# Performance work log

Hardware: AMD Instinct MI355X
Metric: run time of the kernel (lower is better)

The kernel has to match this reference:

```python
import jax, jax.numpy as jnp
import numpy as np

# ---- static config (MaskedViTConfig, eval mode with inference_topk) ----
B, IMG, P, C = 32, 224, 16, 3
G = IMG // P            # 14
N = G * G + 1           # 197 tokens incl cls
D, NH = 768, 12
HD = D // NH            # 64
SCALE = HD ** -0.5
HID = 4 * D             # 3072
GH = 128                # gate hidden
WARM, DYN = 2, 10
TOPK = 118              # min(inference_topk, N-1)
NC = 1000
EPS_MASK = 1e-6
LN_EPS = 1e-5


def _ln(x, g, b):
    mu = x.mean(-1, keepdims=True)
    var = ((x - mu) ** 2).mean(-1, keepdims=True)
    return (x - mu) / jnp.sqrt(var + LN_EPS) * g + b


def _attn(x, qkv_w, qkv_b, proj_w, proj_b, add_mask):
    # x: [B,N,D]; add_mask: [B,N] additive logit bias per key, or None
    Bb, Nn, _ = x.shape
    qkv = (x @ qkv_w + qkv_b).reshape(Bb, Nn, 3, NH, HD)
    q, k, v = qkv[:, :, 0], qkv[:, :, 1], qkv[:, :, 2]  # [B,N,H,hd]
    attn = jnp.einsum('bqhd,bkhd->bhqk', q, k) * SCALE
    if add_mask is not None:
        attn = attn + add_mask[:, None, None, :]
    attn = jax.nn.softmax(attn, axis=-1)
    out = jnp.einsum('bhqk,bkhd->bqhd', attn, v).reshape(Bb, Nn, D)
    return out @ proj_w + proj_b


def _mlp(x, w1, b1, w2, b2):
    return jax.nn.gelu(x @ w1 + b1, approximate=False) @ w2 + b2


def setup_inputs() -> dict:
    key = jax.random.key(0)
    ks = iter(jax.random.split(key, 64))
    nrm = lambda shape, s=0.02: jax.random.normal(next(ks), shape, jnp.float32) * s
    z = lambda *shape: jnp.zeros(shape, jnp.float32)
    o = lambda *shape: jnp.ones(shape, jnp.float32)
    inp = {
        'images': jax.random.normal(next(ks), (B, C, IMG, IMG), jnp.float32),
        'patch_w': nrm((D, C, P, P)), 'patch_b': z(D),
        'cls_token': nrm((1, 1, D)), 'pos_embed': nrm((1, N, D)),
        # warmup blocks, stacked on leading axis [WARM,...]
        'w_ln1_g': o(WARM, D), 'w_ln1_b': z(WARM, D),
        'w_qkv_w': nrm((WARM, D, 3 * D)), 'w_qkv_b': z(WARM, 3 * D),
        'w_proj_w': nrm((WARM, D, D)), 'w_proj_b': z(WARM, D),
        'w_ln2_g': o(WARM, D), 'w_ln2_b': z(WARM, D),
        'w_fc1_w': nrm((WARM, D, HID)), 'w_fc1_b': z(WARM, HID),
        'w_fc2_w': nrm((WARM, HID, D)), 'w_fc2_b': z(WARM, D),
        # dynamic masked blocks [DYN,...]
        'd_ln1_g': o(DYN, D), 'd_ln1_b': z(DYN, D),
        'd_qkv_w': nrm((DYN, D, 3 * D)), 'd_qkv_b': z(DYN, 3 * D),
        'd_proj_w': nrm((DYN, D, D)), 'd_proj_b': z(DYN, D),
        'd_ln2_g': o(DYN, D), 'd_ln2_b': z(DYN, D),
        'd_fc1_w': nrm((DYN, D, HID)), 'd_fc1_b': z(DYN, HID),
        'd_fc2_w': nrm((DYN, HID, D)), 'd_fc2_b': z(DYN, D),
        # gate predictor: LayerNorm -> Linear(D,GH) -> GELU -> Linear(GH,1)
        'd_gln_g': o(DYN, D), 'd_gln_b': z(DYN, D),
        'd_gw1': nrm((DYN, D, GH)), 'd_gb1': z(DYN, GH),
        'd_gw2': nrm((DYN, GH, 1)), 'd_gb2': z(DYN, 1),
        # final norm + head
        'norm_g': o(D), 'norm_b': z(D),
        'head_w': nrm((D, NC)), 'head_b': z(NC),
    }
    return inp


def reference(images, patch_w, patch_b, cls_token, pos_embed,
              w_ln1_g, w_ln1_b, w_qkv_w, w_qkv_b, w_proj_w, w_proj_b,
              w_ln2_g, w_ln2_b, w_fc1_w, w_fc1_b, w_fc2_w, w_fc2_b,
              d_ln1_g, d_ln1_b, d_qkv_w, d_qkv_b, d_proj_w, d_proj_b,
              d_ln2_g, d_ln2_b, d_fc1_w, d_fc1_b, d_fc2_w, d_fc2_b,
              d_gln_g, d_gln_b, d_gw1, d_gb1, d_gw2, d_gb2,
              norm_g, norm_b, head_w, head_b):
    Bb = images.shape[0]
    # patch embed: conv with kernel==stride==P is a block reshape + matmul
    x6 = images.reshape(Bb, C, G, P, G, P)
    x = jnp.einsum('bcxpyq,dcpq->bxyd', x6, patch_w).reshape(Bb, G * G, D) + patch_b
    cls = jnp.broadcast_to(cls_token, (Bb, 1, D))
    x = jnp.concatenate([cls, x], axis=1) + pos_embed  # [B,N,D]

    for i in range(WARM):
        x = x + _attn(_ln(x, w_ln1_g[i], w_ln1_b[i]),
                      w_qkv_w[i], w_qkv_b[i], w_proj_w[i], w_proj_b[i], None)
        x = x + _mlp(_ln(x, w_ln2_g[i], w_ln2_b[i]),
                     w_fc1_w[i], w_fc1_b[i], w_fc2_w[i], w_fc2_b[i])

    for j in range(DYN):
        # gate predictor -> logits [B,N]; cls forced kept
        h = _ln(x, d_gln_g[j], d_gln_b[j])
        logits = (jax.nn.gelu(h @ d_gw1[j] + d_gb1[j], approximate=False)
                  @ d_gw2[j] + d_gb2[j]).squeeze(-1)
        logits = logits.at[:, 0].set(1e9)
        # eval-mode top-k keep mask (inference_topk path)
        _, idx = jax.lax.top_k(logits[:, 1:], TOPK)
        m = jnp.zeros_like(logits).at[:, 0].set(1.0)
        m = m.at[jnp.arange(Bb)[:, None], idx + 1].set(1.0)
        add_mask = jnp.log(jnp.clip(m, EPS_MASK, 1.0))
        x = x + _attn(_ln(x, d_ln1_g[j], d_ln1_b[j]),
                      d_qkv_w[j], d_qkv_b[j], d_proj_w[j], d_proj_b[j], add_mask)
        v = _mlp(_ln(x, d_ln2_g[j], d_ln2_b[j]),
                 d_fc1_w[j], d_fc1_b[j], d_fc2_w[j], d_fc2_b[j])
        x = x + v * m[:, :, None]  # gate_mlp_updates=True

    x = _ln(x, norm_g, norm_b)
    return x[:, 0] @ head_w + head_b  # [B, num_classes]
```

## Files before the change

### kernel.cpp

```cpp
#include <hip/hip_runtime.h>
#include <hip/hip_bf16.h>
#include <math.h>


typedef __bf16 bf16_t;
typedef __attribute__((ext_vector_type(8))) __bf16 bf16x8;
typedef __attribute__((ext_vector_type(4))) float f32x4;

#define DI __device__ __forceinline__

constexpr int NB     = 32;
constexpr int NTOK   = 197;
constexpr int DMODEL = 768;
constexpr int NHEAD  = 12;
constexpr int HDIM   = 64;
constexpr int HIDN   = 3072;
constexpr int GHID   = 128;
constexpr int MROWS  = NB * NTOK;
constexpr int PROWS  = NB * 196;
constexpr int NSEL   = 119;
constexpr int MROWSC = NB * NSEL;
constexpr int NLAYER = 12;
constexpr int KTOP   = 118;
constexpr float ATT_SCALE = 0.125f;
constexpr float LNEPS  = 1e-5f;

DI f32x4 mfma16(bf16x8 a, bf16x8 b, f32x4 c) {
    return __builtin_amdgcn_mfma_f32_16x16x32_bf16(a, b, c, 0, 0, 0);
}

DI void gld_lds16(const void* g, void* l) {
    __builtin_amdgcn_global_load_lds(
        (__attribute__((address_space(1))) void*)(g),
        (__attribute__((address_space(3))) void*)(l), 16, 0, 0);
}

enum { EP_BF16 = 0, EP_GELU = 1, EP_RES = 2, EP_F32 = 4 };

template<int MODE, bool GA, bool SC, bool AT, int BN>
__global__ __launch_bounds__(256)
void gemm_bf16(const bf16_t* __restrict__ A, const bf16_t* __restrict__ Wt,
               const float* __restrict__ bias, void* __restrict__ Cout,
               float* __restrict__ resid, const int* __restrict__ rowidx,
               int M, int N, int K, int ldc, int klen)
{
    constexpr int WN = BN / 2;
    constexpr int NF = WN / 16;
    __shared__ __align__(16) bf16_t As[2][128 * 32];
    __shared__ __align__(16) bf16_t Bs[2][BN * 32];
    const int tid  = threadIdx.x;
    const int lane = tid & 63;
    const int wave = tid >> 6;
    const int wm = wave >> 1, wn = wave & 1;
    const int quad = lane >> 4, l16 = lane & 15;
    const int m0 = blockIdx.y * 128;
    const int n0 = blockIdx.x * BN;
    const int koff = AT ? blockIdx.z * klen : 0;

    f32x4 zero4 = {0.f, 0.f, 0.f, 0.f};
    f32x4 acc[4][NF];
#pragma unroll
    for (int i = 0; i < 4; ++i)
#pragma unroll
        for (int j = 0; j < NF; ++j) acc[i][j] = zero4;

    const int rh  = tid >> 2;
    const int seg = tid & 3;
    int cA0 = min(m0 + rh,      M - 1);
    int cA1 = min(m0 + 64 + rh, M - 1);
    const int rA0 = GA ? rowidx[cA0] : cA0;
    const int rA1 = GA ? rowidx[cA1] : cA1;
    const int rB0 = min(n0 + rh, N - 1);
    const int rB1 = (BN == 128) ? min(n0 + 64 + rh, N - 1) : 0;
    const bf16_t* pA0 = A  + (size_t)rA0 * K + koff + seg * 8;
    const bf16_t* pA1 = A  + (size_t)rA1 * K + koff + seg * 8;
    const bf16_t* pB0 = Wt + (size_t)rB0 * K + koff + seg * 8;
    const bf16_t* pB1 = Wt + (size_t)rB1 * K + koff + seg * 8;
    const int lofs0 = wave * 512;
    const int lofs1 = 2048 + wave * 512;

    auto stage = [&](int kt2, int buf) {
        const int kb = kt2 << 5;
        gld_lds16(pA0 + kb, As[buf] + lofs0);
        gld_lds16(pA1 + kb, As[buf] + lofs1);
        gld_lds16(pB0 + kb, Bs[buf] + lofs0);
        if (BN == 128) gld_lds16(pB1 + kb, Bs[buf] + lofs1);
    };

    const int nkt = klen >> 5;
    stage(0, 0);
    stage(1, 1);

    for (int kt = 0; kt < nkt; ++kt) {
        const int cur = kt & 1;
        if (kt + 1 < nkt) {
            if constexpr (BN == 128) asm volatile("s_waitcnt vmcnt(4)" ::: "memory");
            else                     asm volatile("s_waitcnt vmcnt(3)" ::: "memory");
        } else {
            asm volatile("s_waitcnt vmcnt(0)" ::: "memory");
        }
        __builtin_amdgcn_s_barrier();

        bf16x8 af[4], bfr[NF];
#pragma unroll
        for (int i = 0; i < 4; ++i)
            af[i] = *reinterpret_cast<const bf16x8*>(As[cur] + (wm * 64 + i * 16 + l16) * 32 + quad * 8);
#pragma unroll
        for (int j = 0; j < NF; ++j)
            bfr[j] = *reinterpret_cast<const bf16x8*>(Bs[cur] + (wn * WN + j * 16 + l16) * 32 + quad * 8);

        asm volatile("s_waitcnt lgkmcnt(0)" ::: "memory");
        __builtin_amdgcn_sched_barrier(0);
        __builtin_amdgcn_s_barrier();

        if (kt + 2 < nkt) stage(kt + 2, cur);

#pragma unroll
        for (int i = 0; i < 4; ++i)
#pragma unroll
            for (int j = 0; j < NF; ++j)
                acc[i][j] = mfma16(af[i], bfr[j], acc[i][j]);
    }

    const bool addb = bias && (!AT || blockIdx.z == 0);
#pragma unroll
    for (int j = 0; j < NF; ++j) {
        int c = n0 + wn * WN + j * 16 + l16;
        if (c >= N) continue;
        float bj = addb ? bias[c] : 0.f;
#pragma unroll
        for (int i = 0; i < 4; ++i) {
#pragma unroll
            for (int r = 0; r < 4; ++r) {
                int mr = m0 + wm * 64 + i * 16 + quad * 4 + r;
                if (mr >= M) continue;
                float v = acc[i][j][r] + bj;
                int orow = SC ? rowidx[mr] : mr;
                size_t off = (size_t)orow * ldc + c;
                if (MODE == EP_BF16) {
                    ((bf16_t*)Cout)[off] = (bf16_t)v;
                } else if (MODE == EP_GELU) {
                    float g = 0.5f * v * (1.f + erff(v * 0.70710678118f));
                    ((bf16_t*)Cout)[off] = (bf16_t)g;
                } else if (MODE == EP_F32) {
                    ((float*)Cout)[off] = v;
                } else {
                    if (AT) atomicAdd(&resid[off], v);
                    else    resid[off] += v;
                }
            }
        }
    }
}

DI float block_reduce_sum(float val, float* sh) {
#pragma unroll
    for (int off = 32; off; off >>= 1) val += __shfl_down(val, off, 64);
    __syncthreads();
    if ((threadIdx.x & 63) == 0) sh[threadIdx.x >> 6] = val;
    __syncthreads();
    return sh[0] + sh[1] + sh[2] + sh[3];
}

template<typename OUT>
__global__ __launch_bounds__(256)
void ln_kernel(const float* __restrict__ X, const float* __restrict__ g,
               const float* __restrict__ bta, OUT* __restrict__ H, int row_mul)
{
    __shared__ float sh[4];
    const int t = threadIdx.x;
    const float* xr = X + (size_t)blockIdx.x * row_mul * DMODEL;
    float v[3];
#pragma unroll
    for (int i = 0; i < 3; ++i) v[i] = xr[t + i * 256];
    float s = v[0] + v[1] + v[2];
    s = block_reduce_sum(s, sh);
    float mu = s * (1.f / DMODEL);
    float q = 0.f;
#pragma unroll
    for (int i = 0; i < 3; ++i) { float d = v[i] - mu; q += d * d; }
    q = block_reduce_sum(q, sh);
    float rstd = rsqrtf(q * (1.f / DMODEL) + LNEPS);
    OUT* hr = H + (size_t)blockIdx.x * DMODEL;
#pragma unroll
    for (int i = 0; i < 3; ++i) {
        int c = t + i * 256;
        hr[c] = (OUT)((v[i] - mu) * rstd * g[c] + bta[c]);
    }
}

__global__ __launch_bounds__(256)
void ln_dual_kernel(const float* __restrict__ X,
                    const float* __restrict__ g1, const float* __restrict__ b1,
                    const float* __restrict__ g2, const float* __restrict__ b2,
                    float* __restrict__ H1, bf16_t* __restrict__ H2)
{
    __shared__ float sh[4];
    const int t = threadIdx.x;
    const float* xr = X + (size_t)blockIdx.x * DMODEL;
    float v[3];
#pragma unroll
    for (int i = 0; i < 3; ++i) v[i] = xr[t + i * 256];
    float s = v[0] + v[1] + v[2];
    s = block_reduce_sum(s, sh);
    float mu = s * (1.f / DMODEL);
    float q = 0.f;
#pragma unroll
    for (int i = 0; i < 3; ++i) { float d = v[i] - mu; q += d * d; }
    q = block_reduce_sum(q, sh);
    float rstd = rsqrtf(q * (1.f / DMODEL) + LNEPS);
    float* h1 = H1 + (size_t)blockIdx.x * DMODEL;
    bf16_t* h2 = H2 + (size_t)blockIdx.x * DMODEL;
#pragma unroll
    for (int i = 0; i < 3; ++i) {
        int c = t + i * 256;
        float nrm = (v[i] - mu) * rstd;
        h1[c] = nrm * g1[c] + b1[c];
        h2[c] = (bf16_t)(nrm * g2[c] + b2[c]);
    }
}

template<bool COMPACT>
__global__ __launch_bounds__(256)
void attn_kernel(const bf16_t* __restrict__ qkv,
                 const int* __restrict__ rowidx,
                 bf16_t* __restrict__ outp)
{
    constexpr int NV  = COMPACT ? NSEL : NTOK;
    constexpr int NK  = COMPACT ? 128 : 224;
    constexpr int NKT = COMPACT ? 8 : 13;
    constexpr int NKS = NK / 32;
    constexpr int KP  = NK + 8;
    __shared__ __align__(16) bf16_t Vt[64 * KP];
    __shared__ __align__(16) bf16_t Ps[4][16 * KP];
    const int b = blockIdx.z, h = blockIdx.y, qt = blockIdx.x;
    const int tid = threadIdx.x, wave = tid >> 6, lane = tid & 63;
    const int quad = lane >> 4, l16 = lane & 15;

    {
        int d = tid & 63, ng = tid >> 6;
        for (int n = ng; n < NK; n += 4) {
            bf16_t v = (bf16_t)0.f;
            if (n < NV) {
                size_t row = COMPACT ? (size_t)rowidx[b * NSEL + n]
                                     : (size_t)b * NTOK + n;
                v = qkv[(row * 3 + 2) * DMODEL + h * HDIM + d];
            }
            Vt[d * KP + n] = v;
        }
    }
    __syncthreads();

    const int qbase = qt * 64 + wave * 16;
    const int qrow = qbase + l16;
    const int qc = qrow < 196 ? qrow : 196;
    bf16x8 aq[2];
#pragma unroll
    for (int t = 0; t < 2; ++t)
        aq[t] = *reinterpret_cast<const bf16x8*>(
            qkv + (((size_t)b * NTOK + qc) * 3 + 0) * DMODEL + h * HDIM + t * 32 + quad * 8);

    float sreg[NKT][4];
#pragma unroll
    for (int kt = 0; kt < NKT; ++kt) {
        int key = kt * 16 + l16;
        int kc = key < NV ? key : NV - 1;
        size_t krow = COMPACT ? (size_t)rowidx[b * NSEL + kc]
                              : (size_t)b * NTOK + kc;
        const bf16_t* kb = qkv + (krow * 3 + 1) * DMODEL + h * HDIM;
        bf16x8 kf0 = *reinterpret_cast<const bf16x8*>(kb + quad * 8);
        bf16x8 kf1 = *reinterpret_cast<const bf16x8*>(kb + 32 + quad * 8);
        f32x4 s = {0.f, 0.f, 0.f, 0.f};
        s = mfma16(aq[0], kf0, s);
        s = mfma16(aq[1], kf1, s);
        bool kvalid = key < NV;
#pragma unroll
        for (int r = 0; r < 4; ++r)
            sreg[kt][r] = kvalid ? (s[r] * ATT_SCALE) : -1e30f;
    }

    float psum[4];
#pragma unroll
    for (int r = 0; r < 4; ++r) {
        float mx = -1e30f;
#pragma unroll
        for (int kt = 0; kt < NKT; ++kt) mx = fmaxf(mx, sreg[kt][r]);
#pragma unroll
        for (int d = 1; d < 16; d <<= 1) mx = fmaxf(mx, __shfl_xor(mx, d, 64));
        float sum = 0.f;
#pragma unroll
        for (int kt = 0; kt < NKT; ++kt) {
            float p = expf(sreg[kt][r] - mx);
            sreg[kt][r] = p;
            sum += p;
        }
#pragma unroll
        for (int d = 1; d < 16; d <<= 1) sum += __shfl_xor(sum, d, 64);
        psum[r] = sum;
    }

#pragma unroll
    for (int kt = 0; kt < NKT; ++kt)
#pragma unroll
        for (int r = 0; r < 4; ++r)
            Ps[wave][(quad * 4 + r) * KP + kt * 16 + l16] = (bf16_t)sreg[kt][r];
    if (!COMPACT) {
        int rr = lane & 15, c0 = 208 + (lane >> 4) * 4;
#pragma unroll
        for (int i = 0; i < 4; ++i) Ps[wave][rr * KP + c0 + i] = (bf16_t)0.f;
    }
    __syncthreads();

    f32x4 o[4];
#pragma unroll
    for (int j = 0; j < 4; ++j) o[j] = (f32x4){0.f, 0.f, 0.f, 0.f};
#pragma unroll
    for (int ks = 0; ks < NKS; ++ks) {
        bf16x8 ap = *reinterpret_cast<const bf16x8*>(&Ps[wave][l16 * KP + ks * 32 + quad * 8]);
#pragma unroll
        for (int j = 0; j < 4; ++j) {
            bf16x8 vf = *reinterpret_cast<const bf16x8*>(&Vt[(j * 16 + l16) * KP + ks * 32 + quad * 8]);
            o[j] = mfma16(ap, vf, o[j]);
        }
    }

#pragma unroll
    for (int r = 0; r < 4; ++r) {
        int q = qbase + quad * 4 + r;
        if (q < 197) {
            float rs = 1.f / fmaxf(psum[r], 1e-20f);
#pragma unroll
            for (int j = 0; j < 4; ++j)
                outp[((size_t)b * NTOK + q) * DMODEL + h * HDIM + j * 16 + l16] =
                    (bf16_t)(o[j][r] * rs);
        }
    }
}

__global__ __launch_bounds__(256)
void transpose_f32(const float* __restrict__ src, bf16_t* __restrict__ dst, int K, int N)
{
    __shared__ bf16_t tile[64][65];
    const size_t ls = (size_t)K * N * blockIdx.z;
    int k0 = blockIdx.y * 64, n0 = blockIdx.x * 64;
    int c = threadIdx.x & 63, r0 = threadIdx.x >> 6;
#pragma unroll
    for (int i = 0; i < 16; ++i) {
        int r = r0 + i * 4;
        tile[r][c] = (k0 + r < K && n0 + c < N)
                   ? (bf16_t)src[ls + (size_t)(k0 + r) * N + n0 + c] : (bf16_t)0.f;
    }
    __syncthreads();
#pragma unroll
    for (int i = 0; i < 16; ++i) {
        int r = r0 + i * 4;
        if (n0 + r < N && k0 + c < K) dst[ls + (size_t)(n0 + r) * K + k0 + c] = tile[c][r];
    }
}

__global__ void cvt_f32_bf16(const float* __restrict__ src, bf16_t* __restrict__ dst, int n)
{
    int i = blockIdx.x * 256 + threadIdx.x;
    if (i < n) dst[i] = (bf16_t)src[i];
}

__global__ void im2col_kernel(const float* __restrict__ img, bf16_t* __restrict__ Ap)
{
    int idx = blockIdx.x * 256 + threadIdx.x;
    if (idx >= PROWS * 768) return;
    int col = idx % 768, row = idx / 768;
    int b = row / 196, t = row % 196;
    int gi = t / 14, gj = t % 14;
    int c = col >> 8, rr = col & 255, p = rr >> 4, q = rr & 15;
    Ap[idx] = (bf16_t)img[(((size_t)b * 3 + c) * 224 + gi * 16 + p) * 224 + gj * 16 + q];
}

__global__ void assemble_x(const float* __restrict__ patch, const float* __restrict__ cls,
                           const float* __restrict__ pos, float* __restrict__ X)
{
    int idx = blockIdx.x * 256 + threadIdx.x;
    if (idx >= MROWS * DMODEL) return;
    int d = idx % DMODEL, rest = idx / DMODEL;
    int n = rest % NTOK, b = rest / NTOK;
    float v;
    if (n == 0) v = cls[d] + pos[d];
    else        v = patch[((size_t)b * 196 + (n - 1)) * DMODEL + d] + pos[(size_t)n * DMODEL + d];
    X[idx] = v;
}

__global__ __launch_bounds__(256)
void gate_fused_f32(const float* __restrict__ A, const float* __restrict__ W1,
                    const float* __restrict__ b1, const float* __restrict__ w2,
                    const float* __restrict__ b2, float* __restrict__ logits)
{
    __shared__ __align__(16) float As[16][64];
    __shared__ __align__(16) float Ws[64][128];
    const int tid = threadIdx.x;
    const int m0 = blockIdx.x * 16;
    const int tx = tid & 31;
    const int rg = tid >> 5;
    f32x4 acc0 = {0.f, 0.f, 0.f, 0.f};
    f32x4 acc1 = {0.f, 0.f, 0.f, 0.f};
    for (int k0 = 0; k0 < 768; k0 += 64) {
        __syncthreads();
        {
            int idx = tid * 4;
            int r = idx >> 6, c = idx & 63;
            *reinterpret_cast<f32x4*>(&As[r][c]) =
                *reinterpret_cast<const f32x4*>(&A[(size_t)(m0 + r) * 768 + k0 + c]);
        }
#pragma unroll
        for (int i = 0; i < 8; ++i) {
            int idx = (tid + i * 256) * 4;
            int r = idx >> 7, c = idx & 127;
            *reinterpret_cast<f32x4*>(&Ws[r][c]) =
                *reinterpret_cast<const f32x4*>(&W1[(size_t)(k0 + r) * 128 + c]);
        }
        __syncthreads();
#pragma unroll
        for (int kk = 0; kk < 64; ++kk) {
            float a0 = As[rg * 2 + 0][kk];
            float a1 = As[rg * 2 + 1][kk];
            f32x4 w = *reinterpret_cast<const f32x4*>(&Ws[kk][tx * 4]);
#pragma unroll
            for (int j = 0; j < 4; ++j) {
                acc0[j] += a0 * w[j];
                acc1[j] += a1 * w[j];
            }
        }
    }
    float s0 = 0.f, s1 = 0.f;
#pragma unroll
    for (int j = 0; j < 4; ++j) {
        int c = tx * 4 + j;
        float bj = b1[c], wj = w2[c];
        float v0 = acc0[j] + bj;
        float v1 = acc1[j] + bj;
        s0 += 0.5f * v0 * (1.f + erff(v0 * 0.70710678118f)) * wj;
        s1 += 0.5f * v1 * (1.f + erff(v1 * 0.70710678118f)) * wj;
    }
#pragma unroll
    for (int d = 1; d < 32; d <<= 1) {
        s0 += __shfl_xor(s0, d, 64);
        s1 += __shfl_xor(s1, d, 64);
    }
    if (tx == 0) {
        logits[m0 + rg * 2 + 0] = s0 + b2[0];
        logits[m0 + rg * 2 + 1] = s1 + b2[0];
    }
}

__global__ __launch_bounds__(256)
void topk_kernel(const float* __restrict__ logits, int* __restrict__ rowidx)
{
    __shared__ float ls[196];
    int b = blockIdx.x, t = threadIdx.x;
    if (t < 196) ls[t] = logits[b * NTOK + 1 + t];
    __syncthreads();
    if (t < 196) {
        float li = ls[t];
        int cnt = 0;
        for (int j = 0; j < 196; ++j) {
            float lj = ls[j];
            cnt += (lj > li) || (lj == li && j < t);
        }
        if (cnt < KTOP) rowidx[b * NSEL + 1 + cnt] = b * NTOK + 1 + t;
    }
    if (t == 0) rowidx[b * NSEL] = b * NTOK;
}

__global__ void fill_sentinel(float* out, int n)
{
    int i = blockIdx.x * 256 + threadIdx.x;
    if (i < n) out[i] = 12345.0f;
}

static void launch_gemm(int mode, const bf16_t* A, const bf16_t* Wt, const float* bias,
                        void* C, float* resid,
                        int M, int N, int K, int ldc, hipStream_t s)
{
    dim3 grid((N + 127) / 128, (M + 127) / 128);
    dim3 blk(256);
    switch (mode) {
    case EP_BF16: gemm_bf16<EP_BF16, false, false, false, 128><<<grid, blk, 0, s>>>(A, Wt, bias, C, resid, nullptr, M, N, K, ldc, K); break;
    case EP_GELU: gemm_bf16<EP_GELU, false, false, false, 128><<<grid, blk, 0, s>>>(A, Wt, bias, C, resid, nullptr, M, N, K, ldc, K); break;
    case EP_RES:  gemm_bf16<EP_RES,  false, false, false, 128><<<grid, blk, 0, s>>>(A, Wt, bias, C, resid, nullptr, M, N, K, ldc, K); break;
    case EP_F32:  gemm_bf16<EP_F32,  false, false, false, 128><<<grid, blk, 0, s>>>(A, Wt, bias, C, resid, nullptr, M, N, K, ldc, K); break;
    }
}

static void launch_gemm_res_sk2_n64(const bf16_t* A, const bf16_t* Wt, const float* bias,
                                    float* resid, int M, int N, int K, int ldc, hipStream_t s)
{
    dim3 grid((N + 63) / 64, (M + 127) / 128, 2);
    gemm_bf16<EP_RES, false, false, true, 64><<<grid, 256, 0, s>>>(
        A, Wt, bias, nullptr, resid, nullptr, M, N, K, ldc, K / 2);
}

extern "C" void kernel_launch(void* const* d_in, const int* in_sizes, int n_in,
                              void* d_out, int out_size, void* d_ws, size_t ws_size,
                              hipStream_t stream)
{
    (void)in_sizes; (void)n_in;
    const float* images   = (const float*)d_in[0];
    const float* patch_w  = (const float*)d_in[1];
    const float* patch_b  = (const float*)d_in[2];
    const float* cls_tok  = (const float*)d_in[3];
    const float* pos_emb  = (const float*)d_in[4];
    const float* w_ln1_g  = (const float*)d_in[5];
    const float* w_ln1_b  = (const float*)d_in[6];
    const float* w_qkv_w  = (const float*)d_in[7];
    const float* w_qkv_b  = (const float*)d_in[8];
    const float* w_proj_w = (const float*)d_in[9];
    const float* w_proj_b = (const float*)d_in[10];
    const float* w_ln2_g  = (const float*)d_in[11];
    const float* w_ln2_b  = (const float*)d_in[12];
    const float* w_fc1_w  = (const float*)d_in[13];
    const float* w_fc1_b  = (const float*)d_in[14];
    const float* w_fc2_w  = (const float*)d_in[15];
    const float* w_fc2_b  = (const float*)d_in[16];
    const float* d_ln1_g  = (const float*)d_in[17];
    const float* d_ln1_b  = (const float*)d_in[18];
    const float* d_qkv_w  = (const float*)d_in[19];
    const float* d_qkv_b  = (const float*)d_in[20];
    const float* d_proj_w = (const float*)d_in[21];
    const float* d_proj_b = (const float*)d_in[22];
    const float* d_ln2_g  = (const float*)d_in[23];
    const float* d_ln2_b  = (const float*)d_in[24];
    const float* d_fc1_w  = (const float*)d_in[25];
    const float* d_fc1_b  = (const float*)d_in[26];
    const float* d_fc2_w  = (const float*)d_in[27];
    const float* d_fc2_b  = (const float*)d_in[28];
    const float* d_gln_g  = (const float*)d_in[29];
    const float* d_gln_b  = (const float*)d_in[30];
    const float* d_gw1    = (const float*)d_in[31];
    const float* d_gb1    = (const float*)d_in[32];
    const float* d_gw2    = (const float*)d_in[33];
    const float* d_gb2    = (const float*)d_in[34];
    const float* norm_g   = (const float*)d_in[35];
    const float* norm_b   = (const float*)d_in[36];
    const float* head_w   = (const float*)d_in[37];
    const float* head_b   = (const float*)d_in[38];

    char* wp = (char*)d_ws;
    auto alloc = [&](size_t bytes) -> char* {
        char* p = wp; wp += (bytes + 255) & ~(size_t)255; return p;
    };
    bf16_t* wtqkv  = (bf16_t*)alloc((size_t)NLAYER * 2304 * 768 * 2);
    bf16_t* wtproj = (bf16_t*)alloc((size_t)NLAYER * 768 * 768 * 2);
    bf16_t* wtfc1  = (bf16_t*)alloc((size_t)NLAYER * 3072 * 768 * 2);
    bf16_t* wtfc2  = (bf16_t*)alloc((size_t)NLAYER * 768 * 3072 * 2);
    bf16_t* wthead = (bf16_t*)alloc((size_t)1024 * 768 * 2);
    bf16_t* pwbf   = (bf16_t*)alloc((size_t)768 * 768 * 2);
    float*  x      = (float*)alloc((size_t)MROWS * DMODEL * 4);
    bf16_t* h      = (bf16_t*)alloc((size_t)MROWS * DMODEL * 2);
    float*  hgate  = (float*)alloc((size_t)MROWS * DMODEL * 4);
    bf16_t* hcls   = (bf16_t*)alloc((size_t)NB * DMODEL * 2);
    bf16_t* qkvb   = (bf16_t*)alloc((size_t)MROWS * 2304 * 2);
    bf16_t* attno  = (bf16_t*)alloc((size_t)MROWS * DMODEL * 2);
    bf16_t* hid    = (bf16_t*)alloc((size_t)MROWS * HIDN * 2);
    float*  logits = (float*)alloc((size_t)MROWS * 4);
    int*    rowidx = (int*)alloc((size_t)MROWSC * 4);
    size_t used = (size_t)(wp - (char*)d_ws);
    if (used > ws_size) {
        fill_sentinel<<<(out_size + 255) / 256, 256, 0, stream>>>((float*)d_out, out_size);
        return;
    }
    bf16_t* Ap = hid;
    float* patchout = (float*)((char*)hid + (size_t)PROWS * 768 * 2);

    transpose_f32<<<dim3(36, 12, 2),  256, 0, stream>>>(w_qkv_w,  wtqkv,                      768, 2304);
    transpose_f32<<<dim3(36, 12, 10), 256, 0, stream>>>(d_qkv_w,  wtqkv + (size_t)2*2304*768, 768, 2304);
    transpose_f32<<<dim3(12, 12, 2),  256, 0, stream>>>(w_proj_w, wtproj,                     768, 768);
    transpose_f32<<<dim3(12, 12, 10), 256, 0, stream>>>(d_proj_w, wtproj + (size_t)2*768*768, 768, 768);
    transpose_f32<<<dim3(48, 12, 2),  256, 0, stream>>>(w_fc1_w,  wtfc1,                      768, 3072);
    transpose_f32<<<dim3(48, 12, 10), 256, 0, stream>>>(d_fc1_w,  wtfc1 + (size_t)2*3072*768, 768, 3072);
    transpose_f32<<<dim3(12, 48, 2),  256, 0, stream>>>(w_fc2_w,  wtfc2,                      3072, 768);
    transpose_f32<<<dim3(12, 48, 10), 256, 0, stream>>>(d_fc2_w,  wtfc2 + (size_t)2*768*3072, 3072, 768);
    transpose_f32<<<dim3(16, 12, 1),  256, 0, stream>>>(head_w,   wthead,                     768, 1000);
    cvt_f32_bf16<<<(768 * 768 + 255) / 256, 256, 0, stream>>>(patch_w, pwbf, 768 * 768);

    im2col_kernel<<<(PROWS * 768 + 255) / 256, 256, 0, stream>>>(images, Ap);
    launch_gemm(EP_F32, Ap, pwbf, patch_b, patchout, nullptr,
                PROWS, 768, 768, 768, stream);
    assemble_x<<<(MROWS * DMODEL + 255) / 256, 256, 0, stream>>>(patchout, cls_tok, pos_emb, x);

    for (int L = 0; L < NLAYER; ++L) {
        bool warm = (L < 2);
        int li = warm ? L : (L - 2);
        const float* ln1g = warm ? w_ln1_g + li*768 : d_ln1_g + li*768;
        const float* ln1b = warm ? w_ln1_b + li*768 : d_ln1_b + li*768;
        const float* ln2g = warm ? w_ln2_g + li*768 : d_ln2_g + li*768;
        const float* ln2b = warm ? w_ln2_b + li*768 : d_ln2_b + li*768;
        const float* qkvbias  = warm ? w_qkv_b + li*2304 : d_qkv_b + li*2304;
        const float* projbias = warm ? w_proj_b + li*768 : d_proj_b + li*768;
        const float* fc1bias  = warm ? w_fc1_b + (size_t)li*3072 : d_fc1_b + (size_t)li*3072;
        const float* fc2bias  = warm ? w_fc2_b + li*768 : d_fc2_b + li*768;
        const bf16_t* Wq = wtqkv + (size_t)L * 2304 * 768;
        const bf16_t* Wp = wtproj + (size_t)L * 768 * 768;
        const bf16_t* W1 = wtfc1 + (size_t)L * 3072 * 768;
        const bf16_t* W2 = wtfc2 + (size_t)L * 768 * 3072;

        if (!warm) {
            ln_dual_kernel<<<MROWS, 256, 0, stream>>>(
                x, d_gln_g + li*768, d_gln_b + li*768, ln1g, ln1b, hgate, h);
            gate_fused_f32<<<MROWS / 16, 256, 0, stream>>>(
                hgate, d_gw1 + (size_t)li*768*128, d_gb1 + li*128,
                d_gw2 + (size_t)li*128, d_gb2 + li, logits);
            topk_kernel<<<NB, 256, 0, stream>>>(logits, rowidx);
        } else {
            ln_kernel<bf16_t><<<MROWS, 256, 0, stream>>>(x, ln1g, ln1b, h, 1);
        }
        launch_gemm(EP_BF16, h, Wq, qkvbias, qkvb, nullptr,
                    MROWS, 2304, 768, 2304, stream);
        if (warm)
            attn_kernel<false><<<dim3(4, NHEAD, NB), 256, 0, stream>>>(qkvb, nullptr, attno);
        else
            attn_kernel<true><<<dim3(4, NHEAD, NB), 256, 0, stream>>>(qkvb, rowidx, attno);
        launch_gemm_res_sk2_n64(attno, Wp, projbias, x, MROWS, 768, 768, 768, stream);
        ln_kernel<bf16_t><<<MROWS, 256, 0, stream>>>(x, ln2g, ln2b, h, 1);
        if (warm) {
            launch_gemm(EP_GELU, h, W1, fc1bias, hid, nullptr,
                        MROWS, 3072, 768, 3072, stream);
            launch_gemm_res_sk2_n64(hid, W2, fc2bias, x, MROWS, 768, 3072, 768, stream);
        } else {
            dim3 g1(48, (MROWSC + 127) / 128);
            gemm_bf16<EP_GELU, true, false, false, 64><<<g1, 256, 0, stream>>>(
                h, W1, fc1bias, hid, nullptr, rowidx, MROWSC, 3072, 768, 3072, 768);
            dim3 g2(12, (MROWSC + 127) / 128, 2);
            gemm_bf16<EP_RES, false, true, true, 64><<<g2, 256, 0, stream>>>(
                hid, W2, fc2bias, nullptr, x, rowidx, MROWSC, 768, 3072, 768, 1536);
        }
    }

    ln_kernel<bf16_t><<<NB, 256, 0, stream>>>(x, norm_g, norm_b, hcls, NTOK);
    launch_gemm(EP_F32, hcls, wthead, head_b, d_out, nullptr,
                NB, 1000, 768, 1000, stream);
}
```

Measured before the change: 4.440 ms.

## Remap GEMM workgroups across XCDs and fuse gate LayerNorm into gate kernel

The GEMM kernel now remaps its linear workgroup id so that consecutive tiles land on the same XCD, improving L2 reuse of shared A/B tiles on the multi-die MI355X. Separately, the dual LayerNorm kernel no longer writes a full fp32 normalized copy for the gate. It stores per-row mean and rstd, and the gate kernel applies the gate LayerNorm on the fly while loading X. This removes a large fp32 write and read per dynamic layer, at the cost of redundant normalization arithmetic inside the gate kernel.

```diff
diff --git a/kernel.cpp b/kernel.cpp
--- a/kernel.cpp
+++ b/kernel.cpp
@@ -53,8 +53,15 @@
     const int wave = tid >> 6;
     const int wm = wave >> 1, wn = wave & 1;
     const int quad = lane >> 4, l16 = lane & 15;
-    const int m0 = blockIdx.y * 128;
-    const int n0 = blockIdx.x * BN;
+
+    const int nwg  = gridDim.x * gridDim.y;
+    const int wgid = blockIdx.y * gridDim.x + blockIdx.x;
+    const int qc8  = nwg >> 3, r8 = nwg & 7;
+    const int xcd  = wgid & 7, cidx = wgid >> 3;
+    const int newid = (xcd < r8 ? xcd * (qc8 + 1)
+                                : r8 * (qc8 + 1) + (xcd - r8) * qc8) + cidx;
+    const int m0 = (newid / gridDim.x) * 128;
+    const int n0 = (newid % gridDim.x) * BN;
     const int koff = AT ? blockIdx.z * klen : 0;
 
     f32x4 zero4 = {0.f, 0.f, 0.f, 0.f};
@@ -190,10 +197,9 @@
 }
 
 __global__ __launch_bounds__(256)
-void ln_dual_kernel(const float* __restrict__ X,
-                    const float* __restrict__ g1, const float* __restrict__ b1,
-                    const float* __restrict__ g2, const float* __restrict__ b2,
-                    float* __restrict__ H1, bf16_t* __restrict__ H2)
+void ln_stats_kernel(const float* __restrict__ X,
+                     const float* __restrict__ g, const float* __restrict__ bta,
+                     bf16_t* __restrict__ H, float2* __restrict__ stats)
 {
     __shared__ float sh[4];
     const int t = threadIdx.x;
@@ -209,14 +215,12 @@
     for (int i = 0; i < 3; ++i) { float d = v[i] - mu; q += d * d; }
     q = block_reduce_sum(q, sh);
     float rstd = rsqrtf(q * (1.f / DMODEL) + LNEPS);
-    float* h1 = H1 + (size_t)blockIdx.x * DMODEL;
-    bf16_t* h2 = H2 + (size_t)blockIdx.x * DMODEL;
+    if (t == 0) stats[blockIdx.x] = make_float2(mu, rstd);
+    bf16_t* hr = H + (size_t)blockIdx.x * DMODEL;
 #pragma unroll
     for (int i = 0; i < 3; ++i) {
         int c = t + i * 256;
-        float nrm = (v[i] - mu) * rstd;
-        h1[c] = nrm * g1[c] + b1[c];
-        h2[c] = (bf16_t)(nrm * g2[c] + b2[c]);
+        hr[c] = (bf16_t)((v[i] - mu) * rstd * g[c] + bta[c]);
     }
 }
 
@@ -389,9 +393,11 @@
 }
 
 __global__ __launch_bounds__(256)
-void gate_fused_f32(const float* __restrict__ A, const float* __restrict__ W1,
-                    const float* __restrict__ b1, const float* __restrict__ w2,
-                    const float* __restrict__ b2, float* __restrict__ logits)
+void gate_fused_f32(const float* __restrict__ X, const float2* __restrict__ stats,
+                    const float* __restrict__ lng, const float* __restrict__ lnb,
+                    const float* __restrict__ W1, const float* __restrict__ fb1,
+                    const float* __restrict__ w2, const float* __restrict__ b2,
+                    float* __restrict__ logits)
 {
     __shared__ __align__(16) float As[16][64];
     __shared__ __align__(16) float Ws[64][128];
@@ -406,8 +412,16 @@
         {
             int idx = tid * 4;
             int r = idx >> 6, c = idx & 63;
-            *reinterpret_cast<f32x4*>(&As[r][c]) =
-                *reinterpret_cast<const f32x4*>(&A[(size_t)(m0 + r) * 768 + k0 + c]);
+            int row = m0 + r;
+            float2 st = stats[row];
+            f32x4 xv = *reinterpret_cast<const f32x4*>(&X[(size_t)row * 768 + k0 + c]);
+            f32x4 gv = *reinterpret_cast<const f32x4*>(&lng[k0 + c]);
+            f32x4 bv = *reinterpret_cast<const f32x4*>(&lnb[k0 + c]);
+            f32x4 o;
+#pragma unroll
+            for (int j = 0; j < 4; ++j)
+                o[j] = (xv[j] - st.x) * st.y * gv[j] + bv[j];
+            *reinterpret_cast<f32x4*>(&As[r][c]) = o;
         }
 #pragma unroll
         for (int i = 0; i < 8; ++i) {
@@ -433,7 +447,7 @@
 #pragma unroll
     for (int j = 0; j < 4; ++j) {
         int c = tx * 4 + j;
-        float bj = b1[c], wj = w2[c];
+        float bj = fb1[c], wj = w2[c];
         float v0 = acc0[j] + bj;
         float v1 = acc1[j] + bj;
         s0 += 0.5f * v0 * (1.f + erff(v0 * 0.70710678118f)) * wj;
@@ -554,12 +568,12 @@
     bf16_t* pwbf   = (bf16_t*)alloc((size_t)768 * 768 * 2);
     float*  x      = (float*)alloc((size_t)MROWS * DMODEL * 4);
     bf16_t* h      = (bf16_t*)alloc((size_t)MROWS * DMODEL * 2);
-    float*  hgate  = (float*)alloc((size_t)MROWS * DMODEL * 4);
     bf16_t* hcls   = (bf16_t*)alloc((size_t)NB * DMODEL * 2);
     bf16_t* qkvb   = (bf16_t*)alloc((size_t)MROWS * 2304 * 2);
     bf16_t* attno  = (bf16_t*)alloc((size_t)MROWS * DMODEL * 2);
     bf16_t* hid    = (bf16_t*)alloc((size_t)MROWS * HIDN * 2);
     float*  logits = (float*)alloc((size_t)MROWS * 4);
+    float2* stats  = (float2*)alloc((size_t)MROWS * 8);
     int*    rowidx = (int*)alloc((size_t)MROWSC * 4);
     size_t used = (size_t)(wp - (char*)d_ws);
     if (used > ws_size) {
@@ -602,10 +616,10 @@
         const bf16_t* W2 = wtfc2 + (size_t)L * 768 * 3072;
 
         if (!warm) {
-            ln_dual_kernel<<<MROWS, 256, 0, stream>>>(
-                x, d_gln_g + li*768, d_gln_b + li*768, ln1g, ln1b, hgate, h);
+            ln_stats_kernel<<<MROWS, 256, 0, stream>>>(x, ln1g, ln1b, h, stats);
             gate_fused_f32<<<MROWS / 16, 256, 0, stream>>>(
-                hgate, d_gw1 + (size_t)li*768*128, d_gb1 + li*128,
+                x, stats, d_gln_g + li*768, d_gln_b + li*768,
+                d_gw1 + (size_t)li*768*128, d_gb1 + li*128,
                 d_gw2 + (size_t)li*128, d_gb2 + li, logits);
             topk_kernel<<<NB, 256, 0, stream>>>(logits, rowidx);
         } else {
```

Measured after the change: 4.271 ms. 1.04x faster.
